# Kernel optimization log

Hardware: AMD Instinct MI355X
Metric: run time of the kernel (lower is better)

Reference implementation:

```python
import jax, jax.numpy as jnp
import numpy as np

VERIFY_OP = 0  # protocol['operations','verify']
YES = 0        # protocol['concepts','yes']
NO = 1         # protocol['concepts','no']
EMBED_DIM = 16


def _act(x):
    # torch.clamp(x, -1, 5) + 0.1 * x
    return jnp.clip(x, -1.0, 5.0) + 0.1 * x


def setup_inputs() -> dict:
    key = jax.random.key(0)
    ks = jax.random.split(key, 6)
    B, O, Fd, C, L, E = 32, 64, 512, 512, 16, EMBED_DIM
    D2 = 2 * E * E  # 512
    scene = jax.random.normal(ks[0], (B, O, Fd), jnp.float32)
    program_ops = jax.random.randint(ks[1], (B, L), 0, 4)
    program_concepts = jax.random.randint(ks[2], (B, L), 0, C)
    concept_table = jax.random.normal(ks[3], (C, D2), jnp.float32) * 0.02
    feat_W = jax.random.normal(ks[4], (D2, Fd), jnp.float32) * 0.02
    feat_b = jax.random.normal(ks[5], (D2,), jnp.float32) * 0.02
    return {"scene": scene, "program_ops": program_ops,
            "program_concepts": program_concepts, "concept_table": concept_table,
            "feat_W": feat_W, "feat_b": feat_b}


def reference(scene, program_ops, program_concepts, concept_table, feat_W, feat_b):
    B, O, Fd = scene.shape
    C, D2 = concept_table.shape
    E = EMBED_DIM
    sq = E * E
    N = C + O  # num_nodes = max_concepts + num_objects

    # feature_linear on all scenes (all scenes full -> embed_init rows overwritten)
    objects = jnp.einsum('bof,df->bod', scene, feat_W) + feat_b  # [B,O,2sq]
    concepts = jnp.broadcast_to(concept_table[None], (B, C, D2))
    all_nodes = jnp.concatenate([concepts, objects], axis=1)  # [B,N,2sq]
    n1 = all_nodes[..., :sq].reshape(B, N, E, E)
    n2 = all_nodes[..., sq:].reshape(B, N, E, E)
    nodes = jnp.einsum('bnij,bnjk->bnik', n1, n2)  # [B,N,E,E]
    exp_nodes = nodes.reshape(B, N, sq)

    args_emb = concept_table[program_concepts]  # [B,L,2sq]
    L = args_emb.shape[1]
    g1 = args_emb[..., :sq].reshape(B, L, E, E).transpose(1, 0, 2, 3)  # [L,B,E,E]
    g2 = args_emb[..., sq:].reshape(B, L, E, E).transpose(1, 0, 2, 3)
    ops = program_ops.T  # [L,B]

    def step(att, xs):
        a1, a2, op = xs
        # matmul(a1^T, nodes, a2) per node
        wm = jnp.einsum('bji,bnjk,bkl->bnil', a1, nodes, a2).reshape(B, N, sq)
        em = wm * att[:, :, None]
        sim = jnp.einsum('bnd,bmd->bnm', em, exp_nodes)  # [B,N,N]
        if_verify = _act(sim[:, :, YES] - sim[:, :, NO])  # [B,N]
        if_transfer = _act(sim.sum(axis=1))               # [B,N]
        is_verify = (op == VERIFY_OP).astype(att.dtype)[:, None]
        new_att = is_verify * if_verify + (1.0 - is_verify) * if_transfer
        return new_att, new_att

    att0 = jnp.ones((B, N), scene.dtype)
    att, history = jax.lax.scan(step, att0, (g1, g2, ops))
    return jax.nn.log_softmax(att, axis=1), history
```

## Files before the change

kernel.cpp:

```cpp
#include <hip/hip_runtime.h>

#define Bb 32
#define Oo 64
#define FD 512
#define Cc 512
#define Ll 16
#define SQ 256
#define D2 512
#define NN 576
#define QQ 6
#define NPB 96
#define NPW 12
#define STAG 17u

typedef __attribute__((ext_vector_type(8))) short short8v;
typedef __attribute__((ext_vector_type(4))) float f32x4;
typedef unsigned long long u64;

__device__ inline unsigned short bf16_rne(float f) {
  unsigned u = __builtin_bit_cast(unsigned, f);
  unsigned r = (u + 0x7fffu + ((u >> 16) & 1u)) >> 16;
  return (unsigned short)r;
}
__device__ inline float bf16_to_f(unsigned short h) {
  unsigned u = ((unsigned)h) << 16;
  return __builtin_bit_cast(float, u);
}
__device__ inline u64 pack_tag(float v, unsigned tag) {
  return ((u64)__float_as_uint(v) << 32) | (u64)tag;
}

__global__ __launch_bounds__(256) void prep(const float* __restrict__ W,
                                            unsigned short* __restrict__ WH,
                                            unsigned short* __restrict__ WL,
                                            u64* __restrict__ slotG,
                                            u64* __restrict__ slotS) {
  const int gid = blockIdx.x * 256 + threadIdx.x;
#pragma unroll
  for (int k = 0; k < 2; ++k) {
    const int i = gid * 2 + k;
    if (i < Bb * QQ * 2 * SQ)
      __hip_atomic_store(&slotG[i], 0ULL, __ATOMIC_RELAXED, __HIP_MEMORY_SCOPE_AGENT);
  }
  if (gid < Bb * QQ * 2)
    __hip_atomic_store(&slotS[gid], 0ULL, __ATOMIC_RELAXED, __HIP_MEMORY_SCOPE_AGENT);
  const float4 v = ((const float4*)W)[gid];
  float vv[4] = {v.x, v.y, v.z, v.w};
  unsigned short hh[4], ll[4];
#pragma unroll
  for (int j = 0; j < 4; ++j) {
    unsigned short hb = bf16_rne(vv[j]);
    float rem = vv[j] - bf16_to_f(hb);
    hh[j] = hb;
    ll[j] = bf16_rne(rem);
  }
  ushort4 h, lo;
  h.x = hh[0]; h.y = hh[1]; h.z = hh[2]; h.w = hh[3];
  lo.x = ll[0]; lo.y = ll[1]; lo.z = ll[2]; lo.w = ll[3];
  ((ushort4*)WH)[gid] = h;
  ((ushort4*)WL)[gid] = lo;
}

__global__ __launch_bounds__(256) void gemm_nodes(const float* __restrict__ scene,
                                                  const unsigned short* __restrict__ WH,
                                                  const unsigned short* __restrict__ WL,
                                                  const float* __restrict__ bias,
                                                  const float* __restrict__ ct,
                                                  float* __restrict__ cn,
                                                  float* __restrict__ on) {
  __shared__ __align__(16) float sbuf[16 * 529 + 512];
  const int bid = blockIdx.x, tid = threadIdx.x;
  if (bid >= 128) {
    float* ls = sbuf;
    const int c0 = (bid - 128) * 8;
    for (int i = tid; i < 1024; i += 256)
      ((float4*)ls)[i] = ((const float4*)(ct + (size_t)c0 * D2))[i];
    __syncthreads();
    const int n = tid >> 5, sub = tid & 31;
    const float* n1 = &ls[n * 512];
    const float* n2 = &ls[n * 512 + 256];
    float* dst = cn + (size_t)(c0 + n) * SQ + sub * 8;
#pragma unroll
    for (int j = 0; j < 8; ++j) {
      const int e = sub * 8 + j, i = e >> 4, k = e & 15;
      float s = 0.f;
#pragma unroll
      for (int t = 0; t < 16; ++t) s += n1[i * 16 + t] * n2[t * 16 + k];
      dst[j] = s;
    }
    return;
  }
  float (*objLds)[529] = (float(*)[529])sbuf;
  float* biasL = sbuf + 16 * 529;
  const int wave = tid >> 6, lane = tid & 63;
  const int rowbase = bid * 16;
  for (int i = tid; i < 512; i += 256) biasL[i] = bias[i];

  const int ar = lane & 15;
  const int koff = (lane >> 4) * 8;
  const float* Arow = scene + (size_t)(rowbase + ar) * FD;
  const int ncol0 = wave * 128;
  f32x4 acc[8];
#pragma unroll
  for (int i = 0; i < 8; ++i) acc[i] = (f32x4){0.f, 0.f, 0.f, 0.f};

  for (int k0 = 0; k0 < FD; k0 += 32) {
    float a[8];
    *(float4*)&a[0] = *(const float4*)&Arow[k0 + koff];
    *(float4*)&a[4] = *(const float4*)&Arow[k0 + koff + 4];
    short8v ah, al;
#pragma unroll
    for (int j = 0; j < 8; ++j) {
      unsigned short hb = bf16_rne(a[j]);
      float rem = a[j] - bf16_to_f(hb);
      ah[j] = (short)hb;
      al[j] = (short)bf16_rne(rem);
    }
#pragma unroll
    for (int ni = 0; ni < 8; ++ni) {
      const int d = ncol0 + ni * 16 + ar;
      const short8v wh = *(const short8v*)&WH[(size_t)d * FD + k0 + koff];
      const short8v wl = *(const short8v*)&WL[(size_t)d * FD + k0 + koff];
      acc[ni] = __builtin_amdgcn_mfma_f32_16x16x32_bf16(ah, wh, acc[ni], 0, 0, 0);
      acc[ni] = __builtin_amdgcn_mfma_f32_16x16x32_bf16(ah, wl, acc[ni], 0, 0, 0);
      acc[ni] = __builtin_amdgcn_mfma_f32_16x16x32_bf16(al, wh, acc[ni], 0, 0, 0);
    }
  }
  __syncthreads();
  const int crow = (lane >> 4) * 4;
  const int ccol = lane & 15;
#pragma unroll
  for (int ni = 0; ni < 8; ++ni) {
    const int d = ncol0 + ni * 16 + ccol;
    const float bv = biasL[d];
#pragma unroll
    for (int r = 0; r < 4; ++r) objLds[crow + r][d] = acc[ni][r] + bv;
  }
  __syncthreads();
  const int o = tid >> 4, ii = tid & 15;
  float n1r[16];
#pragma unroll
  for (int j = 0; j < 16; ++j) n1r[j] = objLds[o][ii * 16 + j];
  float* dst = on + (size_t)(rowbase + o) * SQ + ii * 16;
#pragma unroll
  for (int k = 0; k < 16; ++k) {
    float s = 0.f;
#pragma unroll
    for (int j = 0; j < 16; ++j) s += n1r[j] * objLds[o][256 + j * 16 + k];
    dst[k] = s;
  }
}

__global__ __launch_bounds__(512) void scan8(const int* __restrict__ ops_p,
                                             const int* __restrict__ pcs,
                                             const float* __restrict__ ct,
                                             const float* __restrict__ cn,
                                             const float* __restrict__ on,
                                             float* __restrict__ out,
                                             u64* __restrict__ slotG,
                                             u64* __restrict__ slotS) {
  const int b = blockIdx.x & 31;
  const int q = blockIdx.x >> 5;
  const int tid = threadIdx.x, wave = tid >> 6, lane = tid & 63;
  __shared__ __align__(16) float ndl[NPB][SQ];
  __shared__ __align__(16) float Gab[Ll][2 * SQ];
  __shared__ __align__(16) float red[8][SQ];
  __shared__ __align__(16) float gbuf[QQ][SQ];
  __shared__ float hist[Ll][NPB];
  __shared__ __align__(16) float Dls[SQ], Mq[SQ], Tt[SQ];
  __shared__ float attL[NPB];
  __shared__ int opsL[Ll], pcsL[Ll];
  __shared__ float sS[1];

  if (tid < Ll) { opsL[tid] = ops_p[b * Ll + tid]; pcsL[tid] = pcs[b * Ll + tid]; }
  const int n0 = q * NPB;
  for (int idx = tid; idx < NPB * 64; idx += 512) {
    const int r = idx >> 6, c4 = idx & 63;
    const int n = n0 + r;
    const float* src = (n < Cc) ? (cn + (size_t)n * SQ)
                                : (on + ((size_t)b * Oo + (n - Cc)) * SQ);
    *(float4*)&ndl[r][c4 * 4] = *(const float4*)(src + c4 * 4);
  }
  if (tid < SQ) Dls[tid] = cn[tid] - cn[SQ + tid];
  if (tid < NPB) attL[tid] = 1.f;
  __syncthreads();
  for (int idx = tid; idx < Ll * 128; idx += 512) {
    const int l = idx >> 7, j = idx & 127;
    *(float4*)&Gab[l][j * 4] = *(const float4*)&ct[(size_t)pcsL[l] * D2 + j * 4];
  }
  __syncthreads();
#pragma unroll
  for (int li = 0; li < 2; ++li) {
    const int l = wave + li * 8;
    if (opsL[l] == 0) {
      float t4[4];
#pragma unroll
      for (int j = 0; j < 4; ++j) {
        const int e = lane * 4 + j, r = e >> 4, c = e & 15;
        float s = 0.f;
#pragma unroll
        for (int t = 0; t < 16; ++t) s += Dls[r * 16 + t] * Gab[l][SQ + c * 16 + t];
        t4[j] = s;
      }
      *(f32x4*)&red[wave][lane * 4] = *(f32x4*)t4;
      asm volatile("s_waitcnt lgkmcnt(0)" ::: "memory");
      __builtin_amdgcn_sched_barrier(0);
      float g4[4];
#pragma unroll
      for (int j = 0; j < 4; ++j) {
        const int e = lane * 4 + j, r = e >> 4, c = e & 15;
        float s = 0.f;
#pragma unroll
        for (int t = 0; t < 16; ++t) s += Gab[l][r * 16 + t] * red[wave][t * 16 + c];
        g4[j] = s;
      }
      *(f32x4*)&Gab[l][lane * 4] = *(f32x4*)g4;
    }
  }
  f32x4 m = (f32x4){0.f, 0.f, 0.f, 0.f};
#pragma unroll
  for (int ni = 0; ni < NPW; ++ni)
    m += *(const f32x4*)&ndl[wave * NPW + ni][lane * 4];
  __syncthreads();

  const int r16 = lane >> 2, c0 = (lane & 3) * 4;
  int tc = 0;
  for (int l = 0; l < Ll; ++l) {
    const bool verify = (opsL[l] == 0);
    if (!verify) {
      const int par = tc & 1;
      ++tc;
      const unsigned tg = (unsigned)(l + 1);
      *(f32x4*)&red[wave][lane * 4] = m;
      __syncthreads();
      if (wave == 0) {
        f32x4 s = (f32x4){0.f, 0.f, 0.f, 0.f};
#pragma unroll
        for (int w = 0; w < 8; ++w) s += *(const f32x4*)&red[w][lane * 4];
        *(f32x4*)&Mq[lane * 4] = s;
        asm volatile("s_waitcnt lgkmcnt(0)" ::: "memory");
        __builtin_amdgcn_sched_barrier(0);
        f32x4 T4 = (f32x4){0.f, 0.f, 0.f, 0.f};
#pragma unroll
        for (int t = 0; t < 16; ++t) {
          const float a1v = Gab[l][t * 16 + r16];
          const f32x4 mv = *(const f32x4*)&Mq[t * 16 + c0];
          T4[0] += a1v * mv[0]; T4[1] += a1v * mv[1];
          T4[2] += a1v * mv[2]; T4[3] += a1v * mv[3];
        }
        *(f32x4*)&Tt[lane * 4] = T4;
        asm volatile("s_waitcnt lgkmcnt(0)" ::: "memory");
        __builtin_amdgcn_sched_barrier(0);
        f32x4 tr[4];
#pragma unroll
        for (int k = 0; k < 4; ++k) tr[k] = *(const f32x4*)&Tt[r16 * 16 + k * 4];
        f32x4 g = (f32x4){0.f, 0.f, 0.f, 0.f};
#pragma unroll
        for (int t = 0; t < 16; ++t) {
          const float trv = tr[t >> 2][t & 3];
          const f32x4 a2v = *(const f32x4*)&Gab[l][SQ + t * 16 + c0];
          g[0] += trv * a2v[0]; g[1] += trv * a2v[1];
          g[2] += trv * a2v[2]; g[3] += trv * a2v[3];
        }
        *(f32x4*)&gbuf[q][lane * 4] = g;
        asm volatile("s_waitcnt lgkmcnt(0)" ::: "memory");
        __builtin_amdgcn_sched_barrier(0);
        u64* myslot = slotG + ((size_t)(b * QQ + q) * 2 + par) * SQ;
#pragma unroll
        for (int j = 0; j < 4; ++j) {
          const float gv = gbuf[q][j * 64 + lane];
          __hip_atomic_store(&myslot[j * 64 + lane], pack_tag(gv, tg),
                             __ATOMIC_RELAXED, __HIP_MEMORY_SCOPE_AGENT);
        }
      } else if (wave <= QQ - 1) {
        const int qq = (q + wave) % QQ;
        const u64* base = slotG + ((size_t)(b * QQ + qq) * 2 + par) * SQ;
        if (lane == 0) {
          while ((unsigned)__hip_atomic_load(base + (SQ - 1), __ATOMIC_RELAXED,
                                             __HIP_MEMORY_SCOPE_AGENT) != tg) {}
        }
        u64 pk[4];
        for (;;) {
#pragma unroll
          for (int j = 0; j < 4; ++j)
            pk[j] = __hip_atomic_load(base + j * 64 + lane, __ATOMIC_RELAXED,
                                      __HIP_MEMORY_SCOPE_AGENT);
          bool ok = true;
#pragma unroll
          for (int j = 0; j < 4; ++j) ok &= ((unsigned)pk[j] == tg);
          if (__all(ok)) break;
        }
#pragma unroll
        for (int j = 0; j < 4; ++j)
          gbuf[qq][j * 64 + lane] = __uint_as_float((unsigned)(pk[j] >> 32));
      }
      __syncthreads();
      f32x4 gg = (f32x4){0.f, 0.f, 0.f, 0.f};
#pragma unroll
      for (int qq = 0; qq < QQ; ++qq) gg += *(const f32x4*)&gbuf[qq][lane * 4];
      f32x4 mn = (f32x4){0.f, 0.f, 0.f, 0.f};
#pragma unroll
      for (int ni = 0; ni < NPW; ++ni) {
        const int nl = wave * NPW + ni;
        const f32x4 v = *(const f32x4*)&ndl[nl][lane * 4];
        float p = v[0] * gg[0] + v[1] * gg[1] + v[2] * gg[2] + v[3] * gg[3];
        p += __shfl_xor(p, 1);  p += __shfl_xor(p, 2);  p += __shfl_xor(p, 4);
        p += __shfl_xor(p, 8);  p += __shfl_xor(p, 16); p += __shfl_xor(p, 32);
        const float na = fminf(fmaxf(p, -1.f), 5.f) + 0.1f * p;
        if (lane == 0) { attL[nl] = na; hist[l][nl] = na; }
        mn[0] += na * v[0]; mn[1] += na * v[1]; mn[2] += na * v[2]; mn[3] += na * v[3];
      }
      m = mn;
    } else {
      const f32x4 g = *(const f32x4*)&Gab[l][lane * 4];
      f32x4 mn = (f32x4){0.f, 0.f, 0.f, 0.f};
#pragma unroll
      for (int ni = 0; ni < NPW; ++ni) {
        const int nl = wave * NPW + ni;
        const f32x4 v = *(const f32x4*)&ndl[nl][lane * 4];
        float p = v[0] * g[0] + v[1] * g[1] + v[2] * g[2] + v[3] * g[3];
        p += __shfl_xor(p, 1);  p += __shfl_xor(p, 2);  p += __shfl_xor(p, 4);
        p += __shfl_xor(p, 8);  p += __shfl_xor(p, 16); p += __shfl_xor(p, 32);
        const float x = attL[nl] * p;
        const float na = fminf(fmaxf(x, -1.f), 5.f) + 0.1f * x;
        if (lane == 0) { attL[nl] = na; hist[l][nl] = na; }
        mn[0] += na * v[0]; mn[1] += na * v[1]; mn[2] += na * v[2]; mn[3] += na * v[3];
      }
      m = mn;
    }
  }
  __syncthreads();

  if (wave == 0) {
    float mv = -1e30f;
    for (int i = lane; i < NPB; i += 64) mv = fmaxf(mv, attL[i]);
    mv = fmaxf(mv, __shfl_xor(mv, 1));  mv = fmaxf(mv, __shfl_xor(mv, 2));
    mv = fmaxf(mv, __shfl_xor(mv, 4));  mv = fmaxf(mv, __shfl_xor(mv, 8));
    mv = fmaxf(mv, __shfl_xor(mv, 16)); mv = fmaxf(mv, __shfl_xor(mv, 32));
    float sv = 0.f;
    for (int i = lane; i < NPB; i += 64) sv += expf(attL[i] - mv);
    sv += __shfl_xor(sv, 1);  sv += __shfl_xor(sv, 2);  sv += __shfl_xor(sv, 4);
    sv += __shfl_xor(sv, 8);  sv += __shfl_xor(sv, 16); sv += __shfl_xor(sv, 32);
    if (lane == 0) {
      __hip_atomic_store(&slotS[(b * QQ + q) * 2 + 0], pack_tag(mv, STAG),
                         __ATOMIC_RELAXED, __HIP_MEMORY_SCOPE_AGENT);
      __hip_atomic_store(&slotS[(b * QQ + q) * 2 + 1], pack_tag(sv, STAG),
                         __ATOMIC_RELAXED, __HIP_MEMORY_SCOPE_AGENT);
    }
    const int role = (lane < QQ) ? 0 : ((lane >= 8 && lane < 8 + QQ) ? 1 : -1);
    const int sidx = (role == 0) ? ((b * QQ + lane) * 2)
                                 : ((role == 1) ? ((b * QQ + (lane - 8)) * 2 + 1) : 0);
    u64 pk;
    for (;;) {
      pk = (role >= 0) ? __hip_atomic_load(&slotS[sidx], __ATOMIC_RELAXED,
                                           __HIP_MEMORY_SCOPE_AGENT)
                       : (u64)STAG;
      if (__all((unsigned)pk == STAG)) break;
    }
    const float v = __uint_as_float((unsigned)(pk >> 32));
    float gM = -1e30f, gT = 0.f;
#pragma unroll
    for (int qq = 0; qq < QQ; ++qq) gM = fmaxf(gM, __shfl(v, qq));
#pragma unroll
    for (int qq = 0; qq < QQ; ++qq)
      gT += __shfl(v, 8 + qq) * expf(__shfl(v, qq) - gM);
    if (lane == 0) sS[0] = gM + logf(gT);
  }
  __syncthreads();
  const float lse = sS[0];
  if (tid < NPB) out[(size_t)b * NN + n0 + tid] = attL[tid] - lse;
  for (int idx = tid; idx < Ll * NPB; idx += 512) {
    const int l = idx / NPB, i = idx - l * NPB;
    out[(size_t)Bb * NN + ((size_t)l * Bb + b) * NN + n0 + i] = hist[l][i];
  }
}

extern "C" void kernel_launch(void* const* d_in, const int* in_sizes, int n_in,
                              void* d_out, int out_size, void* d_ws, size_t ws_size,
                              hipStream_t stream) {
  const float* scene = (const float*)d_in[0];
  const int* ops = (const int*)d_in[1];
  const int* pcs = (const int*)d_in[2];
  const float* ct = (const float*)d_in[3];
  const float* fW = (const float*)d_in[4];
  const float* fb = (const float*)d_in[5];
  float* out = (float*)d_out;
  float* ws = (float*)d_ws;

  float* cn = ws;
  float* on = cn + (size_t)Cc * SQ;
  unsigned short* WH = (unsigned short*)(on + (size_t)Bb * Oo * SQ);
  unsigned short* WL = WH + (size_t)D2 * FD;
  u64* slotG = (u64*)(WL + (size_t)D2 * FD);
  u64* slotS = slotG + (size_t)Bb * QQ * 2 * SQ;

  prep<<<256, 256, 0, stream>>>(fW, WH, WL, slotG, slotS);
  gemm_nodes<<<192, 256, 0, stream>>>(scene, WH, WL, fb, ct, cn, on);
  scan8<<<Bb * QQ, 512, 0, stream>>>(ops, pcs, ct, cn, on, out, slotG, slotS);
}
```

Measured before the change: 141.5 us.

## Replace block barriers in transfer steps with LDS flag handshakes and register attention

Drops the two __syncthreads per transfer step. Waves now signal through per-wave LDS flags: wave 0 waits only on the partial-sum flags and the other waves wait on gather-complete flags. gbuf is double-buffered by parity so a new step can't overwrite data still being read, and attention values stay in registers instead of LDS. The aim is to cut barrier stalls on the serial scan's critical path, at the cost of spin loops on LDS flags and more delicate memory-ordering correctness.

```diff
diff --git a/kernel.cpp b/kernel.cpp
--- a/kernel.cpp
+++ b/kernel.cpp
@@ -165,14 +165,17 @@
   __shared__ __align__(16) float ndl[NPB][SQ];
   __shared__ __align__(16) float Gab[Ll][2 * SQ];
   __shared__ __align__(16) float red[8][SQ];
-  __shared__ __align__(16) float gbuf[QQ][SQ];
+  __shared__ __align__(16) float gbuf[2][QQ][SQ];
   __shared__ float hist[Ll][NPB];
   __shared__ __align__(16) float Dls[SQ], Mq[SQ], Tt[SQ];
   __shared__ float attL[NPB];
   __shared__ int opsL[Ll], pcsL[Ll];
   __shared__ float sS[1];
+  __shared__ unsigned rflag[8], gflag[QQ];
 
   if (tid < Ll) { opsL[tid] = ops_p[b * Ll + tid]; pcsL[tid] = pcs[b * Ll + tid]; }
+  if (tid < 8) rflag[tid] = 0u;
+  if (tid < QQ) gflag[tid] = 0u;
   const int n0 = q * NPB;
   for (int idx = tid; idx < NPB * 64; idx += 512) {
     const int r = idx >> 6, c4 = idx & 63;
@@ -182,7 +185,6 @@
     *(float4*)&ndl[r][c4 * 4] = *(const float4*)(src + c4 * 4);
   }
   if (tid < SQ) Dls[tid] = cn[tid] - cn[SQ + tid];
-  if (tid < NPB) attL[tid] = 1.f;
   __syncthreads();
   for (int idx = tid; idx < Ll * 128; idx += 512) {
     const int l = idx >> 7, j = idx & 127;
@@ -222,6 +224,10 @@
   for (int ni = 0; ni < NPW; ++ni)
     m += *(const f32x4*)&ndl[wave * NPW + ni][lane * 4];
   __syncthreads();
+
+  float att[NPW];
+#pragma unroll
+  for (int ni = 0; ni < NPW; ++ni) att[ni] = 1.f;
 
   const int r16 = lane >> 2, c0 = (lane & 3) * 4;
   int tc = 0;
@@ -231,12 +237,25 @@
       const int par = tc & 1;
       ++tc;
       const unsigned tg = (unsigned)(l + 1);
-      *(f32x4*)&red[wave][lane * 4] = m;
-      __syncthreads();
+      if (wave != 0) {
+        *(f32x4*)&red[wave][lane * 4] = m;
+        asm volatile("s_waitcnt lgkmcnt(0)" ::: "memory");
+        if (lane == 0)
+          __hip_atomic_store(&rflag[wave], tg, __ATOMIC_RELAXED,
+                             __HIP_MEMORY_SCOPE_WORKGROUP);
+      }
       if (wave == 0) {
-        f32x4 s = (f32x4){0.f, 0.f, 0.f, 0.f};
-#pragma unroll
-        for (int w = 0; w < 8; ++w) s += *(const f32x4*)&red[w][lane * 4];
+        for (;;) {
+          unsigned f = (lane >= 1 && lane < 8)
+                           ? __hip_atomic_load(&rflag[lane], __ATOMIC_RELAXED,
+                                               __HIP_MEMORY_SCOPE_WORKGROUP)
+                           : tg;
+          if (__all(f >= tg)) break;
+        }
+        asm volatile("" ::: "memory");
+        f32x4 s = m;
+#pragma unroll
+        for (int w = 1; w < 8; ++w) s += *(const f32x4*)&red[w][lane * 4];
         *(f32x4*)&Mq[lane * 4] = s;
         asm volatile("s_waitcnt lgkmcnt(0)" ::: "memory");
         __builtin_amdgcn_sched_barrier(0);
@@ -262,23 +281,21 @@
           g[0] += trv * a2v[0]; g[1] += trv * a2v[1];
           g[2] += trv * a2v[2]; g[3] += trv * a2v[3];
         }
-        *(f32x4*)&gbuf[q][lane * 4] = g;
+        *(f32x4*)&gbuf[par][q][lane * 4] = g;
         asm volatile("s_waitcnt lgkmcnt(0)" ::: "memory");
-        __builtin_amdgcn_sched_barrier(0);
+        if (lane == 0)
+          __hip_atomic_store(&gflag[0], tg, __ATOMIC_RELAXED,
+                             __HIP_MEMORY_SCOPE_WORKGROUP);
         u64* myslot = slotG + ((size_t)(b * QQ + q) * 2 + par) * SQ;
 #pragma unroll
         for (int j = 0; j < 4; ++j) {
-          const float gv = gbuf[q][j * 64 + lane];
+          const float gv = gbuf[par][q][j * 64 + lane];
           __hip_atomic_store(&myslot[j * 64 + lane], pack_tag(gv, tg),
                              __ATOMIC_RELAXED, __HIP_MEMORY_SCOPE_AGENT);
         }
       } else if (wave <= QQ - 1) {
         const int qq = (q + wave) % QQ;
         const u64* base = slotG + ((size_t)(b * QQ + qq) * 2 + par) * SQ;
-        if (lane == 0) {
-          while ((unsigned)__hip_atomic_load(base + (SQ - 1), __ATOMIC_RELAXED,
-                                             __HIP_MEMORY_SCOPE_AGENT) != tg) {}
-        }
         u64 pk[4];
         for (;;) {
 #pragma unroll
@@ -292,12 +309,23 @@
         }
 #pragma unroll
         for (int j = 0; j < 4; ++j)
-          gbuf[qq][j * 64 + lane] = __uint_as_float((unsigned)(pk[j] >> 32));
-      }
-      __syncthreads();
+          gbuf[par][qq][j * 64 + lane] = __uint_as_float((unsigned)(pk[j] >> 32));
+        asm volatile("s_waitcnt lgkmcnt(0)" ::: "memory");
+        if (lane == 0)
+          __hip_atomic_store(&gflag[wave], tg, __ATOMIC_RELAXED,
+                             __HIP_MEMORY_SCOPE_WORKGROUP);
+      }
+      for (;;) {
+        unsigned f = (lane < QQ)
+                         ? __hip_atomic_load(&gflag[lane], __ATOMIC_RELAXED,
+                                             __HIP_MEMORY_SCOPE_WORKGROUP)
+                         : tg;
+        if (__all(f >= tg)) break;
+      }
+      asm volatile("" ::: "memory");
       f32x4 gg = (f32x4){0.f, 0.f, 0.f, 0.f};
 #pragma unroll
-      for (int qq = 0; qq < QQ; ++qq) gg += *(const f32x4*)&gbuf[qq][lane * 4];
+      for (int qq = 0; qq < QQ; ++qq) gg += *(const f32x4*)&gbuf[par][qq][lane * 4];
       f32x4 mn = (f32x4){0.f, 0.f, 0.f, 0.f};
 #pragma unroll
       for (int ni = 0; ni < NPW; ++ni) {
@@ -307,7 +335,8 @@
         p += __shfl_xor(p, 1);  p += __shfl_xor(p, 2);  p += __shfl_xor(p, 4);
         p += __shfl_xor(p, 8);  p += __shfl_xor(p, 16); p += __shfl_xor(p, 32);
         const float na = fminf(fmaxf(p, -1.f), 5.f) + 0.1f * p;
-        if (lane == 0) { attL[nl] = na; hist[l][nl] = na; }
+        att[ni] = na;
+        if (lane == 0) hist[l][nl] = na;
         mn[0] += na * v[0]; mn[1] += na * v[1]; mn[2] += na * v[2]; mn[3] += na * v[3];
       }
       m = mn;
@@ -321,13 +350,18 @@
         float p = v[0] * g[0] + v[1] * g[1] + v[2] * g[2] + v[3] * g[3];
         p += __shfl_xor(p, 1);  p += __shfl_xor(p, 2);  p += __shfl_xor(p, 4);
         p += __shfl_xor(p, 8);  p += __shfl_xor(p, 16); p += __shfl_xor(p, 32);
-        const float x = attL[nl] * p;
+        const float x = att[ni] * p;
         const float na = fminf(fmaxf(x, -1.f), 5.f) + 0.1f * x;
-        if (lane == 0) { attL[nl] = na; hist[l][nl] = na; }
+        att[ni] = na;
+        if (lane == 0) hist[l][nl] = na;
         mn[0] += na * v[0]; mn[1] += na * v[1]; mn[2] += na * v[2]; mn[3] += na * v[3];
       }
       m = mn;
     }
+  }
+  if (lane == 0) {
+#pragma unroll
+    for (int ni = 0; ni < NPW; ++ni) attL[wave * NPW + ni] = att[ni];
   }
   __syncthreads();
 
```

Result: slower. 146.3 us (+3.4%).

## Fuse node construction GEMM into scan kernel, compute nodes in place

Applied to the files above, without the earlier changes.

Removes the separate gemm_nodes kernel and its workspace round trip. Each scan block now computes its own node matrices: concept-node products from the concept table in LDS chunks, and for the last block group (q==5) the object feature GEMM via bf16-split MFMA plus the 16x16 product. Shared memory is pooled and aliased to fit the staging buffers. This saves a launch and global traffic, but concept products are recomputed redundantly across the 32 batch blocks, and the q==5 blocks take on the whole per-batch GEMM, which may imbalance the critical path before the synchronized scan.

```diff
diff --git a/kernel.cpp b/kernel.cpp
--- a/kernel.cpp
+++ b/kernel.cpp
@@ -61,128 +61,148 @@
   ((ushort4*)WL)[gid] = lo;
 }
 
-__global__ __launch_bounds__(256) void gemm_nodes(const float* __restrict__ scene,
-                                                  const unsigned short* __restrict__ WH,
-                                                  const unsigned short* __restrict__ WL,
-                                                  const float* __restrict__ bias,
-                                                  const float* __restrict__ ct,
-                                                  float* __restrict__ cn,
-                                                  float* __restrict__ on) {
-  __shared__ __align__(16) float sbuf[16 * 529 + 512];
-  const int bid = blockIdx.x, tid = threadIdx.x;
-  if (bid >= 128) {
-    float* ls = sbuf;
-    const int c0 = (bid - 128) * 8;
-    for (int i = tid; i < 1024; i += 256)
-      ((float4*)ls)[i] = ((const float4*)(ct + (size_t)c0 * D2))[i];
-    __syncthreads();
-    const int n = tid >> 5, sub = tid & 31;
-    const float* n1 = &ls[n * 512];
-    const float* n2 = &ls[n * 512 + 256];
-    float* dst = cn + (size_t)(c0 + n) * SQ + sub * 8;
-#pragma unroll
-    for (int j = 0; j < 8; ++j) {
-      const int e = sub * 8 + j, i = e >> 4, k = e & 15;
-      float s = 0.f;
-#pragma unroll
-      for (int t = 0; t < 16; ++t) s += n1[i * 16 + t] * n2[t * 16 + k];
-      dst[j] = s;
-    }
-    return;
-  }
-  float (*objLds)[529] = (float(*)[529])sbuf;
-  float* biasL = sbuf + 16 * 529;
-  const int wave = tid >> 6, lane = tid & 63;
-  const int rowbase = bid * 16;
-  for (int i = tid; i < 512; i += 256) biasL[i] = bias[i];
-
-  const int ar = lane & 15;
-  const int koff = (lane >> 4) * 8;
-  const float* Arow = scene + (size_t)(rowbase + ar) * FD;
-  const int ncol0 = wave * 128;
-  f32x4 acc[8];
-#pragma unroll
-  for (int i = 0; i < 8; ++i) acc[i] = (f32x4){0.f, 0.f, 0.f, 0.f};
-
-  for (int k0 = 0; k0 < FD; k0 += 32) {
-    float a[8];
-    *(float4*)&a[0] = *(const float4*)&Arow[k0 + koff];
-    *(float4*)&a[4] = *(const float4*)&Arow[k0 + koff + 4];
-    short8v ah, al;
-#pragma unroll
-    for (int j = 0; j < 8; ++j) {
-      unsigned short hb = bf16_rne(a[j]);
-      float rem = a[j] - bf16_to_f(hb);
-      ah[j] = (short)hb;
-      al[j] = (short)bf16_rne(rem);
-    }
-#pragma unroll
-    for (int ni = 0; ni < 8; ++ni) {
-      const int d = ncol0 + ni * 16 + ar;
-      const short8v wh = *(const short8v*)&WH[(size_t)d * FD + k0 + koff];
-      const short8v wl = *(const short8v*)&WL[(size_t)d * FD + k0 + koff];
-      acc[ni] = __builtin_amdgcn_mfma_f32_16x16x32_bf16(ah, wh, acc[ni], 0, 0, 0);
-      acc[ni] = __builtin_amdgcn_mfma_f32_16x16x32_bf16(ah, wl, acc[ni], 0, 0, 0);
-      acc[ni] = __builtin_amdgcn_mfma_f32_16x16x32_bf16(al, wh, acc[ni], 0, 0, 0);
-    }
-  }
-  __syncthreads();
-  const int crow = (lane >> 4) * 4;
-  const int ccol = lane & 15;
-#pragma unroll
-  for (int ni = 0; ni < 8; ++ni) {
-    const int d = ncol0 + ni * 16 + ccol;
-    const float bv = biasL[d];
-#pragma unroll
-    for (int r = 0; r < 4; ++r) objLds[crow + r][d] = acc[ni][r] + bv;
-  }
-  __syncthreads();
-  const int o = tid >> 4, ii = tid & 15;
-  float n1r[16];
-#pragma unroll
-  for (int j = 0; j < 16; ++j) n1r[j] = objLds[o][ii * 16 + j];
-  float* dst = on + (size_t)(rowbase + o) * SQ + ii * 16;
-#pragma unroll
-  for (int k = 0; k < 16; ++k) {
-    float s = 0.f;
-#pragma unroll
-    for (int j = 0; j < 16; ++j) s += n1r[j] * objLds[o][256 + j * 16 + k];
-    dst[k] = s;
-  }
-}
-
 __global__ __launch_bounds__(512) void scan8(const int* __restrict__ ops_p,
                                              const int* __restrict__ pcs,
                                              const float* __restrict__ ct,
-                                             const float* __restrict__ cn,
-                                             const float* __restrict__ on,
+                                             const float* __restrict__ scene,
+                                             const unsigned short* __restrict__ WH,
+                                             const unsigned short* __restrict__ WL,
+                                             const float* __restrict__ bias,
                                              float* __restrict__ out,
                                              u64* __restrict__ slotG,
                                              u64* __restrict__ slotS) {
   const int b = blockIdx.x & 31;
   const int q = blockIdx.x >> 5;
   const int tid = threadIdx.x, wave = tid >> 6, lane = tid & 63;
-  __shared__ __align__(16) float ndl[NPB][SQ];
-  __shared__ __align__(16) float Gab[Ll][2 * SQ];
-  __shared__ __align__(16) float red[8][SQ];
-  __shared__ __align__(16) float gbuf[QQ][SQ];
-  __shared__ float hist[Ll][NPB];
-  __shared__ __align__(16) float Dls[SQ], Mq[SQ], Tt[SQ];
-  __shared__ float attL[NPB];
+  __shared__ __align__(16) float pool[38752];
+  float (*ndl)[SQ]     = (float(*)[SQ])pool;
+  float (*Gab)[2 * SQ] = (float(*)[2 * SQ])(pool + 24576);
+  float (*red)[SQ]     = (float(*)[SQ])(pool + 32768);
+  float (*gbuf)[SQ]    = (float(*)[SQ])(pool + 34816);
+  float (*hist)[NPB]   = (float(*)[NPB])(pool + 36352);
+  float* Dls  = pool + 37888;
+  float* Mq   = pool + 38144;
+  float* Tt   = pool + 38400;
+  float* attL = pool + 38656;
+  float* ctS  = pool + 24576;
+  float (*objLds)[532] = (float(*)[532])(pool + 24576);
+  float* biasL = pool + 34816;
   __shared__ int opsL[Ll], pcsL[Ll];
   __shared__ float sS[1];
 
   if (tid < Ll) { opsL[tid] = ops_p[b * Ll + tid]; pcsL[tid] = pcs[b * Ll + tid]; }
+  if (tid < NPB) attL[tid] = 1.f;
   const int n0 = q * NPB;
-  for (int idx = tid; idx < NPB * 64; idx += 512) {
-    const int r = idx >> 6, c4 = idx & 63;
-    const int n = n0 + r;
-    const float* src = (n < Cc) ? (cn + (size_t)n * SQ)
-                                : (on + ((size_t)b * Oo + (n - Cc)) * SQ);
-    *(float4*)&ndl[r][c4 * 4] = *(const float4*)(src + c4 * 4);
-  }
-  if (tid < SQ) Dls[tid] = cn[tid] - cn[SQ + tid];
-  if (tid < NPB) attL[tid] = 1.f;
+  const int nn = tid >> 5, sub = tid & 31, i2 = sub >> 1, kb = (sub & 1) * 8;
+
+  const int nch = (q < 5) ? 6 : 2;
+  for (int ch = 0; ch < nch; ++ch) {
+    __syncthreads();
+    for (int i = tid; i < 2048; i += 512)
+      ((float4*)ctS)[i] = ((const float4*)(ct + (size_t)(n0 + ch * 16) * D2))[i];
+    __syncthreads();
+    const float* n1p = ctS + nn * 512;
+    const float* n2p = n1p + 256;
+    float n1r[16];
+#pragma unroll
+    for (int k = 0; k < 4; ++k)
+      *(f32x4*)&n1r[k * 4] = *(const f32x4*)&n1p[i2 * 16 + k * 4];
+    f32x4 s0 = (f32x4){0.f, 0.f, 0.f, 0.f}, s1 = (f32x4){0.f, 0.f, 0.f, 0.f};
+#pragma unroll
+    for (int t = 0; t < 16; ++t) {
+      const float w = n1r[t];
+      const f32x4 v0 = *(const f32x4*)&n2p[t * 16 + kb];
+      const f32x4 v1 = *(const f32x4*)&n2p[t * 16 + kb + 4];
+      s0[0] += w * v0[0]; s0[1] += w * v0[1]; s0[2] += w * v0[2]; s0[3] += w * v0[3];
+      s1[0] += w * v1[0]; s1[1] += w * v1[1]; s1[2] += w * v1[2]; s1[3] += w * v1[3];
+    }
+    *(f32x4*)&ndl[ch * 16 + nn][i2 * 16 + kb] = s0;
+    *(f32x4*)&ndl[ch * 16 + nn][i2 * 16 + kb + 4] = s1;
+  }
+  __syncthreads();
+  for (int i = tid; i < 256; i += 512)
+    ((float4*)ctS)[i] = ((const float4*)ct)[i];
+  __syncthreads();
+  if (tid < SQ) {
+    const int ii = tid >> 4, kk = tid & 15;
+    float p0 = 0.f, p1 = 0.f;
+#pragma unroll
+    for (int t = 0; t < 16; ++t) {
+      p0 += ctS[ii * 16 + t] * ctS[256 + t * 16 + kk];
+      p1 += ctS[512 + ii * 16 + t] * ctS[768 + t * 16 + kk];
+    }
+    Dls[tid] = p0 - p1;
+  }
+  if (q == 5) {
+    __syncthreads();
+    biasL[tid] = bias[tid];
+    const int ar = lane & 15, koff = (lane >> 4) * 8;
+    const int ncol0 = wave * 64;
+    f32x4 acc[4][4];
+#pragma unroll
+    for (int rt = 0; rt < 4; ++rt)
+#pragma unroll
+      for (int ni = 0; ni < 4; ++ni) acc[rt][ni] = (f32x4){0.f, 0.f, 0.f, 0.f};
+    for (int k0 = 0; k0 < FD; k0 += 32) {
+      short8v ah[4], al[4];
+#pragma unroll
+      for (int rt = 0; rt < 4; ++rt) {
+        const float* Arow = scene + (size_t)(b * Oo + rt * 16 + ar) * FD;
+        float a[8];
+        *(float4*)&a[0] = *(const float4*)&Arow[k0 + koff];
+        *(float4*)&a[4] = *(const float4*)&Arow[k0 + koff + 4];
+#pragma unroll
+        for (int j = 0; j < 8; ++j) {
+          unsigned short hb = bf16_rne(a[j]);
+          float rem = a[j] - bf16_to_f(hb);
+          ah[rt][j] = (short)hb;
+          al[rt][j] = (short)bf16_rne(rem);
+        }
+      }
+#pragma unroll
+      for (int ni = 0; ni < 4; ++ni) {
+        const int d = ncol0 + ni * 16 + ar;
+        const short8v wh = *(const short8v*)&WH[(size_t)d * FD + k0 + koff];
+        const short8v wl = *(const short8v*)&WL[(size_t)d * FD + k0 + koff];
+#pragma unroll
+        for (int rt = 0; rt < 4; ++rt) {
+          acc[rt][ni] = __builtin_amdgcn_mfma_f32_16x16x32_bf16(ah[rt], wh, acc[rt][ni], 0, 0, 0);
+          acc[rt][ni] = __builtin_amdgcn_mfma_f32_16x16x32_bf16(ah[rt], wl, acc[rt][ni], 0, 0, 0);
+          acc[rt][ni] = __builtin_amdgcn_mfma_f32_16x16x32_bf16(al[rt], wh, acc[rt][ni], 0, 0, 0);
+        }
+      }
+    }
+    const int crow = (lane >> 4) * 4, ccol = lane & 15;
+#pragma unroll
+    for (int g = 0; g < 4; ++g) {
+      __syncthreads();
+#pragma unroll
+      for (int ni = 0; ni < 4; ++ni) {
+        const int d = ncol0 + ni * 16 + ccol;
+        const float bv = biasL[d];
+#pragma unroll
+        for (int r = 0; r < 4; ++r) objLds[crow + r][d] = acc[g][ni][r] + bv;
+      }
+      __syncthreads();
+      const float* n1p = &objLds[nn][0];
+      const float* n2p = n1p + 256;
+      float n1r[16];
+#pragma unroll
+      for (int k = 0; k < 4; ++k)
+        *(f32x4*)&n1r[k * 4] = *(const f32x4*)&n1p[i2 * 16 + k * 4];
+      f32x4 s0 = (f32x4){0.f, 0.f, 0.f, 0.f}, s1 = (f32x4){0.f, 0.f, 0.f, 0.f};
+#pragma unroll
+      for (int t = 0; t < 16; ++t) {
+        const float w = n1r[t];
+        const f32x4 v0 = *(const f32x4*)&n2p[t * 16 + kb];
+        const f32x4 v1 = *(const f32x4*)&n2p[t * 16 + kb + 4];
+        s0[0] += w * v0[0]; s0[1] += w * v0[1]; s0[2] += w * v0[2]; s0[3] += w * v0[3];
+        s1[0] += w * v1[0]; s1[1] += w * v1[1]; s1[2] += w * v1[2]; s1[3] += w * v1[3];
+      }
+      *(f32x4*)&ndl[32 + g * 16 + nn][i2 * 16 + kb] = s0;
+      *(f32x4*)&ndl[32 + g * 16 + nn][i2 * 16 + kb + 4] = s1;
+    }
+  }
   __syncthreads();
   for (int idx = tid; idx < Ll * 128; idx += 512) {
     const int l = idx >> 7, j = idx & 127;
@@ -262,13 +282,13 @@
           g[0] += trv * a2v[0]; g[1] += trv * a2v[1];
           g[2] += trv * a2v[2]; g[3] += trv * a2v[3];
         }
-        *(f32x4*)&gbuf[q][lane * 4] = g;
+        *(f32x4*)&gbuf[0][lane * 4] = g;
         asm volatile("s_waitcnt lgkmcnt(0)" ::: "memory");
         __builtin_amdgcn_sched_barrier(0);
         u64* myslot = slotG + ((size_t)(b * QQ + q) * 2 + par) * SQ;
 #pragma unroll
         for (int j = 0; j < 4; ++j) {
-          const float gv = gbuf[q][j * 64 + lane];
+          const float gv = gbuf[0][j * 64 + lane];
           __hip_atomic_store(&myslot[j * 64 + lane], pack_tag(gv, tg),
                              __ATOMIC_RELAXED, __HIP_MEMORY_SCOPE_AGENT);
         }
@@ -292,7 +312,7 @@
         }
 #pragma unroll
         for (int j = 0; j < 4; ++j)
-          gbuf[qq][j * 64 + lane] = __uint_as_float((unsigned)(pk[j] >> 32));
+          gbuf[wave][j * 64 + lane] = __uint_as_float((unsigned)(pk[j] >> 32));
       }
       __syncthreads();
       f32x4 gg = (f32x4){0.f, 0.f, 0.f, 0.f};
@@ -385,16 +405,12 @@
   const float* fW = (const float*)d_in[4];
   const float* fb = (const float*)d_in[5];
   float* out = (float*)d_out;
-  float* ws = (float*)d_ws;
-
-  float* cn = ws;
-  float* on = cn + (size_t)Cc * SQ;
-  unsigned short* WH = (unsigned short*)(on + (size_t)Bb * Oo * SQ);
+
+  unsigned short* WH = (unsigned short*)d_ws;
   unsigned short* WL = WH + (size_t)D2 * FD;
   u64* slotG = (u64*)(WL + (size_t)D2 * FD);
   u64* slotS = slotG + (size_t)Bb * QQ * 2 * SQ;
 
   prep<<<256, 256, 0, stream>>>(fW, WH, WL, slotG, slotS);
-  gemm_nodes<<<192, 256, 0, stream>>>(scene, WH, WL, fb, ct, cn, on);
-  scan8<<<Bb * QQ, 512, 0, stream>>>(ops, pcs, ct, cn, on, out, slotG, slotS);
-}
+  scan8<<<Bb * QQ, 512, 0, stream>>>(ops, pcs, ct, scene, WH, WL, fb, out, slotG, slotS);
+}
```

Result: slower. 157.4 us (+11.3%).
